# Performance work log

Measured on AMD Instinct MI355X. Metric: run time of the kernel, lower is better.

The kernel has to match this reference:

```python
import jax, jax.numpy as jnp
import numpy as np

N = 100000
E = 1600000
D = 128


def setup_inputs() -> dict:
    key = jax.random.key(0)
    ks = jax.random.split(key, 8)
    x = jax.random.normal(ks[0], (N, D), dtype=jnp.float32)
    edge_index = jax.random.randint(ks[1], (2, E), 0, N, dtype=jnp.int64)
    # Xavier-uniform linear weights, zero-ish biases (PyTorch default bias is uniform; keep small random)
    def xavier(k, fan_in, fan_out):
        limit = float(np.sqrt(6.0 / (fan_in + fan_out)))
        return jax.random.uniform(k, (fan_out, fan_in), minval=-limit, maxval=limit, dtype=jnp.float32)
    W1 = xavier(ks[2], D, D); b1 = jnp.zeros((D,), jnp.float32)
    W2 = xavier(ks[3], D, D); b2 = jnp.zeros((D,), jnp.float32)
    W3 = xavier(ks[4], D, D); b3 = jnp.zeros((D,), jnp.float32)
    return {"x": x, "edge_index": edge_index, "W1": W1, "b1": b1,
            "W2": W2, "b2": b2, "W3": W3, "b3": b3}


def reference(x, edge_index, W1, b1, W2, b2, W3, b3):
    n = x.shape[0]
    loop = jnp.arange(n, dtype=edge_index.dtype)
    row = jnp.concatenate([edge_index[0], loop])  # source (x_j index)
    col = jnp.concatenate([edge_index[1], loop])  # target (aggregation index)
    # degree over row after self-loops; every node appears at least once
    deg = jax.ops.segment_sum(jnp.ones_like(row, dtype=x.dtype), row, num_segments=n)
    dis = deg ** -0.5
    norm = dis[row] * dis[col]  # [E+N]

    def gconv(h, W, b):
        h = h @ W.T + b                      # linear projection [N, D]
        msg = norm[:, None] * h[row]         # gather + elementwise norm [E+N, D]
        return jax.ops.segment_sum(msg, col, num_segments=n)  # scatter-add

    h = jax.nn.relu(gconv(x, W1, b1))
    h = jax.nn.relu(gconv(h, W2, b2))
    h = jax.nn.relu(gconv(h, W3, b3))
    return h
```

## Files before the change

### kernel.cpp

```cpp
#include <hip/hip_runtime.h>
#include <hip/hip_fp16.h>

#define THREADS 256
#define ELL 64
#define EPT 4
#define RSIZE 16384
#define NSLICE 64

typedef _Float16 f16x8 __attribute__((ext_vector_type(8)));
typedef float f32x4 __attribute__((ext_vector_type(4)));

__device__ inline uint2 pack_half4(float4 v) {
    __half2 a = __floats2half2_rn(v.x, v.y);
    __half2 b = __floats2half2_rn(v.z, v.w);
    uint2 o;
    o.x = *reinterpret_cast<unsigned int*>(&a);
    o.y = *reinterpret_cast<unsigned int*>(&b);
    return o;
}
__device__ inline float4 unpack_half4(uint2 v) {
    __half2 a = *reinterpret_cast<__half2*>(&v.x);
    __half2 b = *reinterpret_cast<__half2*>(&v.y);
    float2 f0 = __half22float2(a);
    float2 f1 = __half22float2(b);
    return make_float4(f0.x, f0.y, f1.x, f1.y);
}


__global__ void preinit_kernel(const int* __restrict__ ei, int* __restrict__ flag,
                               int* __restrict__ fill, int* __restrict__ csr, int n) {
    int i = blockIdx.x * blockDim.x + threadIdx.x;
    if (i == 0) {
        int nz = 0;
        for (int k = 1; k < 256; k += 2) nz |= ei[k];
        *flag = (nz == 0) ? 1 : 0;
    }
    if (i < n) {
        fill[i] = 1;
        csr[(size_t)i * ELL] = i;
    }
}

__global__ __launch_bounds__(THREADS) void fused_pre_kernel(
    const int* __restrict__ ei, const int* __restrict__ flag,
    int* __restrict__ ghist, int* __restrict__ fill, int* __restrict__ csr,
    const float4* __restrict__ x, uint2* __restrict__ h16,
    const float* __restrict__ w0, const float* __restrict__ w1,
    const float* __restrict__ w2, _Float16* __restrict__ wfbuf,
    int eN, int n, int nA, int nB, int nC) {
    __shared__ unsigned int lh[RSIZE / 2];
    const int bid = blockIdx.x;
    const int tid = threadIdx.x;

    if (bid < nA) {
        const int g = bid / NSLICE, s = bid % NSLICE;
        for (int i = tid; i < RSIZE / 2; i += THREADS) lh[i] = 0;
        __syncthreads();
        const int lo = (int)((long long)eN * s / NSLICE);
        const int hi = (int)((long long)eN * (s + 1) / NSLICE);
        const int rbase = g * RSIZE;
        if (*flag) {
            const long long* e64 = (const long long*)ei;
            for (int idx = lo + tid; idx < hi; idx += THREADS) {
                unsigned int local = (unsigned int)((int)e64[idx] - rbase);
                if (local < RSIZE)
                    atomicAdd(&lh[local >> 1], 1u << ((local & 1) << 4));
            }
        } else {
            for (int idx = lo + tid; idx < hi; idx += THREADS) {
                unsigned int local = (unsigned int)(ei[idx] - rbase);
                if (local < RSIZE)
                    atomicAdd(&lh[local >> 1], 1u << ((local & 1) << 4));
            }
        }
        __syncthreads();
        for (int i = tid; i < RSIZE; i += THREADS) {
            int node = rbase + i;
            if (node < n)
                ghist[(size_t)s * n + node] =
                    (int)((lh[i >> 1] >> ((i & 1) << 4)) & 0xFFFFu);
        }
    } else if (bid < nA + nB) {
        const int t = (bid - nA) * THREADS + tid;
        const int base = t * EPT;
        if (base >= eN) return;
        int r[EPT], c[EPT];
        const int m = min(EPT, eN - base);
        if (*flag) {
            const long long* e64 = (const long long*)ei;
#pragma unroll
            for (int k = 0; k < EPT; ++k)
                if (k < m) { r[k] = (int)e64[base + k]; c[k] = (int)e64[eN + base + k]; }
        } else {
#pragma unroll
            for (int k = 0; k < EPT; ++k)
                if (k < m) { r[k] = ei[base + k]; c[k] = ei[eN + base + k]; }
        }
        int pos[EPT];
#pragma unroll
        for (int k = 0; k < EPT; ++k)
            if (k < m) pos[k] = atomicAdd(&fill[c[k]], 1);
#pragma unroll
        for (int k = 0; k < EPT; ++k)
            if (k < m) csr[(size_t)c[k] * ELL + pos[k]] = r[k];
    } else if (bid < nA + nB + nC) {
        const int total = n * 32;
        for (int i = (bid - nA - nB) * THREADS + tid; i < total; i += nC * THREADS)
            h16[i] = pack_half4(x[i]);
    } else {
        const int i = (bid - nA - nB - nC) * THREADS + tid;
        if (i < 3 * 8 * 4 * 64) {
            int lane = i & 63;
            int kt = (i >> 6) & 3;
            int nt = (i >> 8) & 7;
            int l  = i >> 11;
            const float* w = (l == 0) ? w0 : (l == 1) ? w1 : w2;
            int o  = nt * 16 + (lane & 15);
            int kb = kt * 32 + (lane >> 4) * 8;
            _Float16* dst = wfbuf + (size_t)i * 8;
#pragma unroll
            for (int j = 0; j < 8; ++j) dst[j] = (_Float16)w[o * 128 + kb + j];
        }
    }
}

__global__ void dis_kernel(const int* __restrict__ ghist, float* __restrict__ dis, int n) {
    int i = blockIdx.x * blockDim.x + threadIdx.x;
    if (i >= n) return;
    int deg = 1;
#pragma unroll 8
    for (int s = 0; s < NSLICE; ++s) deg += ghist[(size_t)s * n + i];
    dis[i] = 1.0f / sqrtf((float)deg);
}

__global__ void sumw_kernel(const int* __restrict__ csr, const int* __restrict__ fill,
                            const float* __restrict__ dis, float* __restrict__ sumw,
                            float* __restrict__ w32, int n) {
    int i = blockIdx.x * blockDim.x + threadIdx.x;
    if (i >= n) return;
    int len = fill[i];
    const int base = i * ELL;
    const float dg = dis[i];
    float t = 0.f;
    for (int j = 0; j < len; ++j) {
        float w = dg * dis[csr[base + j]];
        w32[base + j] = w;
        t += w;
    }
    sumw[i] = t;
}


__global__ void agg_kernel(const uint2* __restrict__ h, const int* __restrict__ csr,
                           const int* __restrict__ fill, const float* __restrict__ w32,
                           uint2* __restrict__ out, int n) {
    const int wid = blockIdx.x * (blockDim.x >> 6) + (threadIdx.x >> 6);
    const int lane = threadIdx.x & 63;
    const int half = lane >> 5;
    const int l32 = lane & 31;
    if (wid >= n) return;
    const int len = fill[wid];
    const int base = wid * ELL;

    float4 a0 = make_float4(0.f, 0.f, 0.f, 0.f);
    float4 a1 = make_float4(0.f, 0.f, 0.f, 0.f);
    float4 a2 = make_float4(0.f, 0.f, 0.f, 0.f);
    float4 a3 = make_float4(0.f, 0.f, 0.f, 0.f);
    int j = half;
    for (; j + 6 < len; j += 8) {
        int u0 = csr[base + j];
        int u1 = csr[base + j + 2];
        int u2 = csr[base + j + 4];
        int u3 = csr[base + j + 6];
        float w0 = w32[base + j];
        float w1 = w32[base + j + 2];
        float w2 = w32[base + j + 4];
        float w3 = w32[base + j + 6];
        float4 v0 = unpack_half4(h[(size_t)u0 * 32 + l32]);
        float4 v1 = unpack_half4(h[(size_t)u1 * 32 + l32]);
        float4 v2 = unpack_half4(h[(size_t)u2 * 32 + l32]);
        float4 v3 = unpack_half4(h[(size_t)u3 * 32 + l32]);
        a0.x = fmaf(w0, v0.x, a0.x); a0.y = fmaf(w0, v0.y, a0.y);
        a0.z = fmaf(w0, v0.z, a0.z); a0.w = fmaf(w0, v0.w, a0.w);
        a1.x = fmaf(w1, v1.x, a1.x); a1.y = fmaf(w1, v1.y, a1.y);
        a1.z = fmaf(w1, v1.z, a1.z); a1.w = fmaf(w1, v1.w, a1.w);
        a2.x = fmaf(w2, v2.x, a2.x); a2.y = fmaf(w2, v2.y, a2.y);
        a2.z = fmaf(w2, v2.z, a2.z); a2.w = fmaf(w2, v2.w, a2.w);
        a3.x = fmaf(w3, v3.x, a3.x); a3.y = fmaf(w3, v3.y, a3.y);
        a3.z = fmaf(w3, v3.z, a3.z); a3.w = fmaf(w3, v3.w, a3.w);
    }
    for (; j < len; j += 2) {
        int u = csr[base + j];
        float w = w32[base + j];
        float4 v = unpack_half4(h[(size_t)u * 32 + l32]);
        a0.x = fmaf(w, v.x, a0.x); a0.y = fmaf(w, v.y, a0.y);
        a0.z = fmaf(w, v.z, a0.z); a0.w = fmaf(w, v.w, a0.w);
    }
    a0.x += a1.x + a2.x + a3.x;
    a0.y += a1.y + a2.y + a3.y;
    a0.z += a1.z + a2.z + a3.z;
    a0.w += a1.w + a2.w + a3.w;

    a0.x += __shfl_xor(a0.x, 32, 64);
    a0.y += __shfl_xor(a0.y, 32, 64);
    a0.z += __shfl_xor(a0.z, 32, 64);
    a0.w += __shfl_xor(a0.w, 32, 64);

    if (half == 0) {
        out[(size_t)wid * 32 + l32] = pack_half4(a0);
    }
}

template <bool OUT16>
__global__ __launch_bounds__(THREADS) void lin_mfma_kernel(
    const _Float16* __restrict__ a16, const _Float16* __restrict__ wfrag,
    const float* __restrict__ bias, const float* __restrict__ sumw,
    float* __restrict__ outf, _Float16* __restrict__ outh, int n) {
    const int lane = threadIdx.x & 63;
    const int g = lane >> 4;
    const int m15 = lane & 15;
    const int wavesPerBlock = blockDim.x >> 6;
    const int wave = blockIdx.x * wavesPerBlock + (threadIdx.x >> 6);
    const int nwaves = gridDim.x * wavesPerBlock;

    f16x8 wf[8][4];
#pragma unroll
    for (int nt = 0; nt < 8; ++nt)
#pragma unroll
        for (int kt = 0; kt < 4; ++kt)
            wf[nt][kt] = *reinterpret_cast<const f16x8*>(
                wfrag + ((size_t)((nt * 4 + kt) * 64 + lane)) * 8);

    const int ntiles = (n + 15) >> 4;
    for (int t = wave; t < ntiles; t += nwaves) {
        const int myrow = t * 16 + m15;
        const int rr = (myrow < n) ? myrow : (n - 1);
        const _Float16* arow = a16 + (size_t)rr * 128 + g * 8;
        f16x8 af[4];
#pragma unroll
        for (int kt = 0; kt < 4; ++kt)
            af[kt] = *reinterpret_cast<const f16x8*>(arow + kt * 32);

        f32x4 acc[8];
#pragma unroll
        for (int nt = 0; nt < 8; ++nt) acc[nt] = (f32x4){0.f, 0.f, 0.f, 0.f};
#pragma unroll
        for (int kt = 0; kt < 4; ++kt)
#pragma unroll
            for (int nt = 0; nt < 8; ++nt)
                acc[nt] = __builtin_amdgcn_mfma_f32_16x16x32_f16(
                    wf[nt][kt], af[kt], acc[nt], 0, 0, 0);

        if (myrow < n) {
            const float sw = sumw[myrow];
#pragma unroll
            for (int nt = 0; nt < 8; ++nt) {
                const float4 b4 = *reinterpret_cast<const float4*>(bias + nt * 16 + g * 4);
                float vx = fmaxf(acc[nt][0] + sw * b4.x, 0.f);
                float vy = fmaxf(acc[nt][1] + sw * b4.y, 0.f);
                float vz = fmaxf(acc[nt][2] + sw * b4.z, 0.f);
                float vw = fmaxf(acc[nt][3] + sw * b4.w, 0.f);
                size_t oidx = (size_t)myrow * 128 + nt * 16 + g * 4;
                if (OUT16) {
                    *reinterpret_cast<uint2*>(outh + oidx) =
                        pack_half4(make_float4(vx, vy, vz, vw));
                } else {
                    *reinterpret_cast<float4*>(outf + oidx) =
                        make_float4(vx, vy, vz, vw);
                }
            }
        }
    }
}


extern "C" void kernel_launch(void* const* d_in, const int* in_sizes, int n_in,
                              void* d_out, int out_size, void* d_ws, size_t ws_size,
                              hipStream_t stream) {
    const float* x  = (const float*)d_in[0];
    const int*   ei = (const int*)d_in[1];
    const float* Ws[3] = {(const float*)d_in[2], (const float*)d_in[4], (const float*)d_in[6]};
    const float* bs[3] = {(const float*)d_in[3], (const float*)d_in[5], (const float*)d_in[7]};
    const int n = in_sizes[0] / 128;
    const int e = in_sizes[1] / 2;

    char* ws = (char*)d_ws;
    size_t cur = 0;
    auto alloc = [&](size_t bytes) {
        void* p = ws + cur;
        cur = (cur + bytes + 255) & ~(size_t)255;
        return p;
    };
    uint2*     A16   = (uint2*)alloc((size_t)n * 128 * 2);
    uint2*     H16   = (uint2*)alloc((size_t)n * 128 * 2);
    int*       csr   = (int*)  alloc((size_t)n * ELL * 4);
    float*     w32   = (float*)alloc((size_t)n * ELL * 4);
    int*       ghist = (int*)  alloc((size_t)NSLICE * n * 4);
    int*       fill  = (int*)  alloc((size_t)n * 4);
    float*     dis   = (float*)alloc((size_t)n * 4);
    float*     sumw  = (float*)alloc((size_t)n * 4);
    _Float16*  wf    = (_Float16*)alloc(3 * 8 * 4 * 64 * 8 * 2);
    int*       flag  = (int*)  alloc(4);

    const int nr = (n + RSIZE - 1) / RSIZE;
    const int nA = nr * NSLICE;
    const int nB = ((e + EPT - 1) / EPT + THREADS - 1) / THREADS;
    const int nC = 256;
    const int nD = (3 * 8 * 4 * 64 + THREADS - 1) / THREADS;

    preinit_kernel<<<(n + 255) / 256, 256, 0, stream>>>(ei, flag, fill, csr, n);
    fused_pre_kernel<<<nA + nB + nC + nD, THREADS, 0, stream>>>(
        ei, flag, ghist, fill, csr, (const float4*)x, H16,
        Ws[0], Ws[1], Ws[2], wf, e, n, nA, nB, nC);
    dis_kernel<<<(n + 255) / 256, 256, 0, stream>>>(ghist, dis, n);
    sumw_kernel<<<(n + 255) / 256, 256, 0, stream>>>(csr, fill, dis, sumw, w32, n);

    for (int l = 0; l < 3; ++l) {
        agg_kernel<<<(n + 3) / 4, 256, 0, stream>>>(
            H16, csr, fill, w32, A16, n);
        const _Float16* wfl = wf + (size_t)l * 8 * 4 * 64 * 8;
        if (l < 2) {
            lin_mfma_kernel<true><<<512, THREADS, 0, stream>>>(
                (const _Float16*)A16, wfl, bs[l], sumw,
                nullptr, (_Float16*)H16, n);
        } else {
            lin_mfma_kernel<false><<<512, THREADS, 0, stream>>>(
                (const _Float16*)A16, wfl, bs[l], sumw,
                (float*)d_out, nullptr, n);
        }
    }
}
```

Before: 451.6 us.

## Bucket neighbor lists by source range and aggregate many nodes per wave

```diff
diff --git a/kernel.cpp b/kernel.cpp
--- a/kernel.cpp
+++ b/kernel.cpp
@@ -6,6 +6,9 @@
 #define EPT 4
 #define RSIZE 16384
 #define NSLICE 64
+#define BSH 13
+#define NB 13
+#define NPW 25
 
 typedef _Float16 f16x8 __attribute__((ext_vector_type(8)));
 typedef float f32x4 __attribute__((ext_vector_type(4)));
@@ -18,13 +21,6 @@
     o.y = *reinterpret_cast<unsigned int*>(&b);
     return o;
 }
-__device__ inline float4 unpack_half4(uint2 v) {
-    __half2 a = *reinterpret_cast<__half2*>(&v.x);
-    __half2 b = *reinterpret_cast<__half2*>(&v.y);
-    float2 f0 = __half22float2(a);
-    float2 f1 = __half22float2(b);
-    return make_float4(f0.x, f0.y, f1.x, f1.y);
-}
 
 
 __global__ void preinit_kernel(const int* __restrict__ ei, int* __restrict__ flag,
@@ -47,7 +43,7 @@
     const float4* __restrict__ x, uint2* __restrict__ h16,
     const float* __restrict__ w0, const float* __restrict__ w1,
     const float* __restrict__ w2, _Float16* __restrict__ wfbuf,
-    int eN, int n, int nA, int nB, int nC) {
+    int eN, int n, int nA, int nB2, int nC) {
     __shared__ unsigned int lh[RSIZE / 2];
     const int bid = blockIdx.x;
     const int tid = threadIdx.x;
@@ -80,7 +76,7 @@
                 ghist[(size_t)s * n + node] =
                     (int)((lh[i >> 1] >> ((i & 1) << 4)) & 0xFFFFu);
         }
-    } else if (bid < nA + nB) {
+    } else if (bid < nA + nB2) {
         const int t = (bid - nA) * THREADS + tid;
         const int base = t * EPT;
         if (base >= eN) return;
@@ -103,12 +99,12 @@
 #pragma unroll
         for (int k = 0; k < EPT; ++k)
             if (k < m) csr[(size_t)c[k] * ELL + pos[k]] = r[k];
-    } else if (bid < nA + nB + nC) {
+    } else if (bid < nA + nB2 + nC) {
         const int total = n * 32;
-        for (int i = (bid - nA - nB) * THREADS + tid; i < total; i += nC * THREADS)
+        for (int i = (bid - nA - nB2) * THREADS + tid; i < total; i += nC * THREADS)
             h16[i] = pack_half4(x[i]);
     } else {
-        const int i = (bid - nA - nB - nC) * THREADS + tid;
+        const int i = (bid - nA - nB2 - nC) * THREADS + tid;
         if (i < 3 * 8 * 4 * 64) {
             int lane = i & 63;
             int kt = (i >> 6) & 3;
@@ -133,81 +129,105 @@
     dis[i] = 1.0f / sqrtf((float)deg);
 }
 
-__global__ void sumw_kernel(const int* __restrict__ csr, const int* __restrict__ fill,
-                            const float* __restrict__ dis, float* __restrict__ sumw,
-                            float* __restrict__ w32, int n) {
+__global__ void bucketize_kernel(const int* __restrict__ csr, const int* __restrict__ fill,
+                                 const float* __restrict__ dis, int* __restrict__ csrB,
+                                 _Float16* __restrict__ w16, uint4* __restrict__ boff,
+                                 float* __restrict__ sumw, int n) {
     int i = blockIdx.x * blockDim.x + threadIdx.x;
     if (i >= n) return;
-    int len = fill[i];
+    const int len = fill[i];
     const int base = i * ELL;
+    unsigned long long c0 = 0, c1 = 0;
+    for (int j = 0; j < len; ++j) {
+        int b = csr[base + j] >> BSH;
+        if (b < 8) c0 += 1ull << (b * 8);
+        else       c1 += 1ull << ((b - 8) * 8);
+    }
+    int ends[NB];
+    int run = 0;
+#pragma unroll
+    for (int b = 0; b < NB; ++b) {
+        int cb = (b < 8) ? (int)((c0 >> (b * 8)) & 255) : (int)((c1 >> ((b - 8) * 8)) & 255);
+        run += cb;
+        ends[b] = run;
+    }
+    uint4 bo;
+    bo.x = (unsigned)ends[0] | ((unsigned)ends[1] << 8) | ((unsigned)ends[2] << 16) | ((unsigned)ends[3] << 24);
+    bo.y = (unsigned)ends[4] | ((unsigned)ends[5] << 8) | ((unsigned)ends[6] << 16) | ((unsigned)ends[7] << 24);
+    bo.z = (unsigned)ends[8] | ((unsigned)ends[9] << 8) | ((unsigned)ends[10] << 16) | ((unsigned)ends[11] << 24);
+    bo.w = (unsigned)ends[12];
+    boff[i] = bo;
+    unsigned long long s0 = 0, s1 = 0;
+#pragma unroll
+    for (int b = 0; b < NB; ++b) {
+        int cb = (b < 8) ? (int)((c0 >> (b * 8)) & 255) : (int)((c1 >> ((b - 8) * 8)) & 255);
+        int st = ends[b] - cb;
+        if (b < 8) s0 |= (unsigned long long)st << (b * 8);
+        else       s1 |= (unsigned long long)st << ((b - 8) * 8);
+    }
     const float dg = dis[i];
     float t = 0.f;
     for (int j = 0; j < len; ++j) {
-        float w = dg * dis[csr[base + j]];
-        w32[base + j] = w;
+        int u = csr[base + j];
+        int b = u >> BSH;
+        int off;
+        if (b < 8) { off = (int)((s0 >> (b * 8)) & 255); s0 += 1ull << (b * 8); }
+        else       { off = (int)((s1 >> ((b - 8) * 8)) & 255); s1 += 1ull << ((b - 8) * 8); }
+        float w = dg * dis[u];
+        csrB[base + off] = u;
+        w16[base + off] = (_Float16)w;
         t += w;
     }
     sumw[i] = t;
 }
 
 
-__global__ void agg_kernel(const uint2* __restrict__ h, const int* __restrict__ csr,
-                           const int* __restrict__ fill, const float* __restrict__ w32,
-                           uint2* __restrict__ out, int n) {
-    const int wid = blockIdx.x * (blockDim.x >> 6) + (threadIdx.x >> 6);
+__global__ __launch_bounds__(THREADS) void agg2_kernel(
+    const unsigned int* __restrict__ h,
+    const int* __restrict__ csrB, const _Float16* __restrict__ w16,
+    const uint4* __restrict__ boff, unsigned int* __restrict__ out, int n) {
     const int lane = threadIdx.x & 63;
-    const int half = lane >> 5;
-    const int l32 = lane & 31;
-    if (wid >= n) return;
-    const int len = fill[wid];
-    const int base = wid * ELL;
-
-    float4 a0 = make_float4(0.f, 0.f, 0.f, 0.f);
-    float4 a1 = make_float4(0.f, 0.f, 0.f, 0.f);
-    float4 a2 = make_float4(0.f, 0.f, 0.f, 0.f);
-    float4 a3 = make_float4(0.f, 0.f, 0.f, 0.f);
-    int j = half;
-    for (; j + 6 < len; j += 8) {
-        int u0 = csr[base + j];
-        int u1 = csr[base + j + 2];
-        int u2 = csr[base + j + 4];
-        int u3 = csr[base + j + 6];
-        float w0 = w32[base + j];
-        float w1 = w32[base + j + 2];
-        float w2 = w32[base + j + 4];
-        float w3 = w32[base + j + 6];
-        float4 v0 = unpack_half4(h[(size_t)u0 * 32 + l32]);
-        float4 v1 = unpack_half4(h[(size_t)u1 * 32 + l32]);
-        float4 v2 = unpack_half4(h[(size_t)u2 * 32 + l32]);
-        float4 v3 = unpack_half4(h[(size_t)u3 * 32 + l32]);
-        a0.x = fmaf(w0, v0.x, a0.x); a0.y = fmaf(w0, v0.y, a0.y);
-        a0.z = fmaf(w0, v0.z, a0.z); a0.w = fmaf(w0, v0.w, a0.w);
-        a1.x = fmaf(w1, v1.x, a1.x); a1.y = fmaf(w1, v1.y, a1.y);
-        a1.z = fmaf(w1, v1.z, a1.z); a1.w = fmaf(w1, v1.w, a1.w);
-        a2.x = fmaf(w2, v2.x, a2.x); a2.y = fmaf(w2, v2.y, a2.y);
-        a2.z = fmaf(w2, v2.z, a2.z); a2.w = fmaf(w2, v2.w, a2.w);
-        a3.x = fmaf(w3, v3.x, a3.x); a3.y = fmaf(w3, v3.y, a3.y);
-        a3.z = fmaf(w3, v3.z, a3.z); a3.w = fmaf(w3, v3.w, a3.w);
-    }
-    for (; j < len; j += 2) {
-        int u = csr[base + j];
-        float w = w32[base + j];
-        float4 v = unpack_half4(h[(size_t)u * 32 + l32]);
-        a0.x = fmaf(w, v.x, a0.x); a0.y = fmaf(w, v.y, a0.y);
-        a0.z = fmaf(w, v.z, a0.z); a0.w = fmaf(w, v.w, a0.w);
-    }
-    a0.x += a1.x + a2.x + a3.x;
-    a0.y += a1.y + a2.y + a3.y;
-    a0.z += a1.z + a2.z + a3.z;
-    a0.w += a1.w + a2.w + a3.w;
-
-    a0.x += __shfl_xor(a0.x, 32, 64);
-    a0.y += __shfl_xor(a0.y, 32, 64);
-    a0.z += __shfl_xor(a0.z, 32, 64);
-    a0.w += __shfl_xor(a0.w, 32, 64);
-
-    if (half == 0) {
-        out[(size_t)wid * 32 + l32] = pack_half4(a0);
+    const int wave = (blockIdx.x * blockDim.x + threadIdx.x) >> 6;
+    const int b0 = wave * NPW;
+
+    float2 acc[NPW];
+#pragma unroll
+    for (int i = 0; i < NPW; ++i) acc[i] = make_float2(0.f, 0.f);
+
+    for (int p = 0; p < NB; ++p) {
+#pragma unroll
+        for (int i = 0; i < NPW; ++i) {
+            const int node = b0 + i;
+            if (node < n) {
+                const uint4 bo = boff[node];
+                unsigned selp = p < 4 ? bo.x : p < 8 ? bo.y : p < 12 ? bo.z : bo.w;
+                int e2 = (int)((selp >> ((p & 3) * 8)) & 255u);
+                int s = 0;
+                if (p > 0) {
+                    int pm = p - 1;
+                    unsigned selm = pm < 4 ? bo.x : pm < 8 ? bo.y : pm < 12 ? bo.z : bo.w;
+                    s = (int)((selm >> ((pm & 3) * 8)) & 255u);
+                }
+                const int segbase = node * ELL;
+                for (int j = s; j < e2; ++j) {
+                    int u = csrB[segbase + j];
+                    float w = (float)w16[segbase + j];
+                    unsigned int hv = h[(size_t)u * 64 + lane];
+                    __half2 hh = *reinterpret_cast<__half2*>(&hv);
+                    float2 v = __half22float2(hh);
+                    acc[i].x = fmaf(w, v.x, acc[i].x);
+                    acc[i].y = fmaf(w, v.y, acc[i].y);
+                }
+            }
+        }
+    }
+#pragma unroll
+    for (int i = 0; i < NPW; ++i) {
+        const int node = b0 + i;
+        if (node < n) {
+            __half2 hh = __floats2half2_rn(acc[i].x, acc[i].y);
+            out[(size_t)node * 64 + lane] = *reinterpret_cast<unsigned int*>(&hh);
+        }
     }
 }
 
@@ -294,8 +314,10 @@
     uint2*     A16   = (uint2*)alloc((size_t)n * 128 * 2);
     uint2*     H16   = (uint2*)alloc((size_t)n * 128 * 2);
     int*       csr   = (int*)  alloc((size_t)n * ELL * 4);
-    float*     w32   = (float*)alloc((size_t)n * ELL * 4);
     int*       ghist = (int*)  alloc((size_t)NSLICE * n * 4);
+    int*       csrB  = ghist;
+    _Float16*  w16   = (_Float16*)alloc((size_t)n * ELL * 2);
+    uint4*     boff  = (uint4*)alloc((size_t)n * 16);
     int*       fill  = (int*)  alloc((size_t)n * 4);
     float*     dis   = (float*)alloc((size_t)n * 4);
     float*     sumw  = (float*)alloc((size_t)n * 4);
@@ -304,20 +326,22 @@
 
     const int nr = (n + RSIZE - 1) / RSIZE;
     const int nA = nr * NSLICE;
-    const int nB = ((e + EPT - 1) / EPT + THREADS - 1) / THREADS;
+    const int nB2 = ((e + EPT - 1) / EPT + THREADS - 1) / THREADS;
     const int nC = 256;
     const int nD = (3 * 8 * 4 * 64 + THREADS - 1) / THREADS;
 
     preinit_kernel<<<(n + 255) / 256, 256, 0, stream>>>(ei, flag, fill, csr, n);
-    fused_pre_kernel<<<nA + nB + nC + nD, THREADS, 0, stream>>>(
+    fused_pre_kernel<<<nA + nB2 + nC + nD, THREADS, 0, stream>>>(
         ei, flag, ghist, fill, csr, (const float4*)x, H16,
-        Ws[0], Ws[1], Ws[2], wf, e, n, nA, nB, nC);
+        Ws[0], Ws[1], Ws[2], wf, e, n, nA, nB2, nC);
     dis_kernel<<<(n + 255) / 256, 256, 0, stream>>>(ghist, dis, n);
-    sumw_kernel<<<(n + 255) / 256, 256, 0, stream>>>(csr, fill, dis, sumw, w32, n);
-
+    bucketize_kernel<<<(n + 255) / 256, 256, 0, stream>>>(
+        csr, fill, dis, csrB, w16, boff, sumw, n);
+
+    const int aggBlocks = (n + NPW * 4 - 1) / (NPW * 4);
     for (int l = 0; l < 3; ++l) {
-        agg_kernel<<<(n + 3) / 4, 256, 0, stream>>>(
-            H16, csr, fill, w32, A16, n);
+        agg2_kernel<<<aggBlocks, THREADS, 0, stream>>>(
+            (const unsigned int*)H16, csrB, w16, boff, (unsigned int*)A16, n);
         const _Float16* wfl = wf + (size_t)l * 8 * 4 * 64 * 8;
         if (l < 2) {
             lin_mfma_kernel<true><<<512, THREADS, 0, stream>>>(
```

New measurement: 1.307 ms. +189.3%, slower.

## Build CSR via per-slice target histograms and LDS-atomic fill instead of global atomics

Applied to the files above, without the earlier changes.

```diff
diff --git a/kernel.cpp b/kernel.cpp
--- a/kernel.cpp
+++ b/kernel.cpp
@@ -3,8 +3,8 @@
 
 #define THREADS 256
 #define ELL 64
-#define EPT 4
 #define RSIZE 16384
+#define RS_F 16384
 #define NSLICE 64
 
 typedef _Float16 f16x8 __attribute__((ext_vector_type(8)));
@@ -28,47 +28,48 @@
 
 
 __global__ void preinit_kernel(const int* __restrict__ ei, int* __restrict__ flag,
-                               int* __restrict__ fill, int* __restrict__ csr, int n) {
+                               int* __restrict__ csr, int n) {
     int i = blockIdx.x * blockDim.x + threadIdx.x;
     if (i == 0) {
         int nz = 0;
         for (int k = 1; k < 256; k += 2) nz |= ei[k];
         *flag = (nz == 0) ? 1 : 0;
     }
-    if (i < n) {
-        fill[i] = 1;
-        csr[(size_t)i * ELL] = i;
-    }
+    if (i < n) csr[(size_t)i * ELL] = i;
 }
 
 __global__ __launch_bounds__(THREADS) void fused_pre_kernel(
     const int* __restrict__ ei, const int* __restrict__ flag,
-    int* __restrict__ ghist, int* __restrict__ fill, int* __restrict__ csr,
+    int* __restrict__ ghist, int* __restrict__ ghistT,
     const float4* __restrict__ x, uint2* __restrict__ h16,
     const float* __restrict__ w0, const float* __restrict__ w1,
     const float* __restrict__ w2, _Float16* __restrict__ wfbuf,
-    int eN, int n, int nA, int nB, int nC) {
+    int eN, int n, int nA, int nC) {
     __shared__ unsigned int lh[RSIZE / 2];
     const int bid = blockIdx.x;
     const int tid = threadIdx.x;
 
-    if (bid < nA) {
-        const int g = bid / NSLICE, s = bid % NSLICE;
+    if (bid < 2 * nA) {
+        const bool tgt = (bid >= nA);
+        const int b = tgt ? bid - nA : bid;
+        const int g = b / NSLICE, s = b % NSLICE;
+        int* gout = tgt ? ghistT : ghist;
         for (int i = tid; i < RSIZE / 2; i += THREADS) lh[i] = 0;
         __syncthreads();
         const int lo = (int)((long long)eN * s / NSLICE);
         const int hi = (int)((long long)eN * (s + 1) / NSLICE);
         const int rbase = g * RSIZE;
+        const int off = tgt ? eN : 0;
         if (*flag) {
             const long long* e64 = (const long long*)ei;
             for (int idx = lo + tid; idx < hi; idx += THREADS) {
-                unsigned int local = (unsigned int)((int)e64[idx] - rbase);
+                unsigned int local = (unsigned int)((int)e64[off + idx] - rbase);
                 if (local < RSIZE)
                     atomicAdd(&lh[local >> 1], 1u << ((local & 1) << 4));
             }
         } else {
             for (int idx = lo + tid; idx < hi; idx += THREADS) {
-                unsigned int local = (unsigned int)(ei[idx] - rbase);
+                unsigned int local = (unsigned int)(ei[off + idx] - rbase);
                 if (local < RSIZE)
                     atomicAdd(&lh[local >> 1], 1u << ((local & 1) << 4));
             }
@@ -77,38 +78,15 @@
         for (int i = tid; i < RSIZE; i += THREADS) {
             int node = rbase + i;
             if (node < n)
-                ghist[(size_t)s * n + node] =
+                gout[(size_t)s * n + node] =
                     (int)((lh[i >> 1] >> ((i & 1) << 4)) & 0xFFFFu);
         }
-    } else if (bid < nA + nB) {
-        const int t = (bid - nA) * THREADS + tid;
-        const int base = t * EPT;
-        if (base >= eN) return;
-        int r[EPT], c[EPT];
-        const int m = min(EPT, eN - base);
-        if (*flag) {
-            const long long* e64 = (const long long*)ei;
-#pragma unroll
-            for (int k = 0; k < EPT; ++k)
-                if (k < m) { r[k] = (int)e64[base + k]; c[k] = (int)e64[eN + base + k]; }
-        } else {
-#pragma unroll
-            for (int k = 0; k < EPT; ++k)
-                if (k < m) { r[k] = ei[base + k]; c[k] = ei[eN + base + k]; }
-        }
-        int pos[EPT];
-#pragma unroll
-        for (int k = 0; k < EPT; ++k)
-            if (k < m) pos[k] = atomicAdd(&fill[c[k]], 1);
-#pragma unroll
-        for (int k = 0; k < EPT; ++k)
-            if (k < m) csr[(size_t)c[k] * ELL + pos[k]] = r[k];
-    } else if (bid < nA + nB + nC) {
+    } else if (bid < 2 * nA + nC) {
         const int total = n * 32;
-        for (int i = (bid - nA - nB) * THREADS + tid; i < total; i += nC * THREADS)
+        for (int i = (bid - 2 * nA) * THREADS + tid; i < total; i += nC * THREADS)
             h16[i] = pack_half4(x[i]);
     } else {
-        const int i = (bid - nA - nB - nC) * THREADS + tid;
+        const int i = (bid - 2 * nA - nC) * THREADS + tid;
         if (i < 3 * 8 * 4 * 64) {
             int lane = i & 63;
             int kt = (i >> 6) & 3;
@@ -131,6 +109,58 @@
 #pragma unroll 8
     for (int s = 0; s < NSLICE; ++s) deg += ghist[(size_t)s * n + i];
     dis[i] = 1.0f / sqrtf((float)deg);
+}
+
+__global__ void scanT_kernel(int* __restrict__ ghistT, int* __restrict__ fill, int n) {
+    int c = blockIdx.x * blockDim.x + threadIdx.x;
+    if (c >= n) return;
+    int running = 1;
+    for (int s = 0; s < NSLICE; ++s) {
+        size_t idx = (size_t)s * n + c;
+        int cnt = ghistT[idx];
+        ghistT[idx] = running;
+        running += cnt;
+    }
+    fill[c] = running;
+}
+
+__global__ __launch_bounds__(THREADS) void fill2_kernel(
+    const int* __restrict__ ei, const int* __restrict__ flag,
+    const int* __restrict__ starts, int* __restrict__ csr, int eN, int n) {
+    __shared__ unsigned int lcur[RS_F];
+    const int s = blockIdx.x % NSLICE;
+    const int g = blockIdx.x / NSLICE;
+    const int rbase = g * RS_F;
+    const int tid = threadIdx.x;
+    for (int i = tid; i < RS_F; i += THREADS) {
+        int node = rbase + i;
+        lcur[i] = (node < n) ? (unsigned int)starts[(size_t)s * n + node] : 0u;
+    }
+    __syncthreads();
+    const int lo = (int)((long long)eN * s / NSLICE);
+    const int hi = (int)((long long)eN * (s + 1) / NSLICE);
+    if (*flag) {
+        const long long* e64 = (const long long*)ei;
+        for (int idx = lo + tid; idx < hi; idx += THREADS) {
+            int c = (int)e64[eN + idx];
+            unsigned int local = (unsigned int)(c - rbase);
+            if (local < RS_F) {
+                int r = (int)e64[idx];
+                unsigned int pos = atomicAdd(&lcur[local], 1u);
+                csr[(size_t)c * ELL + pos] = r;
+            }
+        }
+    } else {
+        for (int idx = lo + tid; idx < hi; idx += THREADS) {
+            int c = ei[eN + idx];
+            unsigned int local = (unsigned int)(c - rbase);
+            if (local < RS_F) {
+                int r = ei[idx];
+                unsigned int pos = atomicAdd(&lcur[local], 1u);
+                csr[(size_t)c * ELL + pos] = r;
+            }
+        }
+    }
 }
 
 __global__ void sumw_kernel(const int* __restrict__ csr, const int* __restrict__ fill,
@@ -295,6 +325,7 @@
     uint2*     H16   = (uint2*)alloc((size_t)n * 128 * 2);
     int*       csr   = (int*)  alloc((size_t)n * ELL * 4);
     float*     w32   = (float*)alloc((size_t)n * ELL * 4);
+    int*       ghistT= (int*)  w32;
     int*       ghist = (int*)  alloc((size_t)NSLICE * n * 4);
     int*       fill  = (int*)  alloc((size_t)n * 4);
     float*     dis   = (float*)alloc((size_t)n * 4);
@@ -304,15 +335,17 @@
 
     const int nr = (n + RSIZE - 1) / RSIZE;
     const int nA = nr * NSLICE;
-    const int nB = ((e + EPT - 1) / EPT + THREADS - 1) / THREADS;
     const int nC = 256;
     const int nD = (3 * 8 * 4 * 64 + THREADS - 1) / THREADS;
-
-    preinit_kernel<<<(n + 255) / 256, 256, 0, stream>>>(ei, flag, fill, csr, n);
-    fused_pre_kernel<<<nA + nB + nC + nD, THREADS, 0, stream>>>(
-        ei, flag, ghist, fill, csr, (const float4*)x, H16,
-        Ws[0], Ws[1], Ws[2], wf, e, n, nA, nB, nC);
+    const int nrF = (n + RS_F - 1) / RS_F;
+
+    preinit_kernel<<<(n + 255) / 256, 256, 0, stream>>>(ei, flag, csr, n);
+    fused_pre_kernel<<<2 * nA + nC + nD, THREADS, 0, stream>>>(
+        ei, flag, ghist, ghistT, (const float4*)x, H16,
+        Ws[0], Ws[1], Ws[2], wf, e, n, nA, nC);
     dis_kernel<<<(n + 255) / 256, 256, 0, stream>>>(ghist, dis, n);
+    scanT_kernel<<<(n + 255) / 256, 256, 0, stream>>>(ghistT, fill, n);
+    fill2_kernel<<<nrF * NSLICE, THREADS, 0, stream>>>(ei, flag, ghistT, csr, e, n);
     sumw_kernel<<<(n + 255) / 256, 256, 0, stream>>>(csr, fill, dis, sumw, w32, n);
 
     for (int l = 0; l < 3; ++l) {
```

New measurement: 429.7 us. -4.9%, faster.
